# Optimization experiments

Hardware: AMD Instinct MI355X
Metric: run time of the kernel (lower is better)

The kernel has to match this reference:

```python
import jax, jax.numpy as jnp
import numpy as np

B, S, D = 2, 2048, 1024
H, E = 16, 64


def setup_inputs() -> dict:
    key = jax.random.key(0)
    k1, k2, k3, k4 = jax.random.split(key, 4)
    x = jax.random.normal(k1, (B, S, D), dtype=jnp.float32)
    # per-head Q/K/V projection weights, stacked over the head axis
    scale = 1.0 / np.sqrt(D)
    Wq = jax.random.normal(k2, (H, D, E), dtype=jnp.float32) * scale
    Wk = jax.random.normal(k3, (H, D, E), dtype=jnp.float32) * scale
    Wv = jax.random.normal(k4, (H, D, E), dtype=jnp.float32) * scale
    return {"x": x, "Wq": Wq, "Wk": Wk, "Wv": Wv}


def reference(x, Wq, Wk, Wv):
    # Grouped-over-heads equivalent of the per-head torch loop.
    q = jnp.einsum("bsd,hde->bhse", x, Wq)  # [B,H,S,E]
    k = jnp.einsum("bsd,hde->bhse", x, Wk)
    v = jnp.einsum("bsd,hde->bhse", x, Wv)

    scores = jnp.einsum("bhse,bhte->bhst", q, k)  # [B,H,S,S]
    scores = scores / jnp.sqrt(jnp.asarray(E, dtype=scores.dtype))
    causal = jnp.tril(jnp.ones((S, S), dtype=bool))  # True on/below diagonal
    scores = jnp.where(causal, scores, jnp.finfo(scores.dtype).min)
    attn = jax.nn.softmax(scores, axis=-1)  # dropout p=0.0 -> identity

    out = jnp.einsum("bhst,bhte->bhse", attn, v)  # [B,H,S,E]
    # concat over heads on the last dim, matching torch.concat(..., dim=-1)
    return out.transpose(0, 2, 1, 3).reshape(B, S, H * E)
```

## Files before the change

kernel.cpp:

```cpp
#include <hip/hip_runtime.h>
#include <stdint.h>

#define S_LEN 2048
#define D_DIM 1024
#define NB 2
#define NH 16
#define NE 64
#define M_ROWS (NB * S_LEN)
#define N_COLS (3 * NH * NE)
#define K_DIM D_DIM

typedef unsigned short u16;
typedef unsigned int u32;
typedef u16 u16x8 __attribute__((ext_vector_type(8)));
typedef __bf16 bf16x8 __attribute__((ext_vector_type(8)));
typedef float f32x4 __attribute__((ext_vector_type(4)));

__device__ __forceinline__ u16 f2b(float f) {
  u32 u = __builtin_bit_cast(u32, f);
  return (u16)((u + 0x7FFFu + ((u >> 16) & 1u)) >> 16);
}

__device__ __forceinline__ void gload_lds16(const void* g, void* l) {
  __builtin_amdgcn_global_load_lds(
      (const __attribute__((address_space(1))) u32*)g,
      (__attribute__((address_space(3))) u32*)l, 16, 0, 0);
}

__global__ __launch_bounds__(256) void k_prep(const float* __restrict__ x,
                                              const float* __restrict__ Wq,
                                              const float* __restrict__ Wk,
                                              const float* __restrict__ Wv,
                                              u16* __restrict__ xb,
                                              u16* __restrict__ Wt) {
  __shared__ u16 tile[64][65];
  int bid = blockIdx.x;
  int t = threadIdx.x;
  if (bid < 2048) {
    size_t i = (size_t)bid * 256 + t;
    const float4* xf = (const float4*)x;
    float4 a = xf[2 * i], c = xf[2 * i + 1];
    u16x8 o;
    o[0] = f2b(a.x); o[1] = f2b(a.y); o[2] = f2b(a.z); o[3] = f2b(a.w);
    o[4] = f2b(c.x); o[5] = f2b(c.y); o[6] = f2b(c.z); o[7] = f2b(c.w);
    *(u16x8*)(xb + 8 * i) = o;
  } else {
    int wbid = bid - 2048;
    int kb = wbid & 15;
    int h = (wbid >> 4) & 15;
    int proj = wbid >> 8;
    const float* W = (proj == 0) ? Wq : ((proj == 1) ? Wk : Wv);
    int k0 = kb * 64;
    int e = t & 63, kr = t >> 6;
    const float* src = W + ((size_t)h * D_DIM + k0 + kr * 16) * NE + e;
#pragma unroll
    for (int j = 0; j < 16; ++j) tile[kr * 16 + j][e] = f2b(src[(size_t)j * NE]);
    __syncthreads();
    int e2 = t >> 2, kc = (t & 3) * 16;
    u16x8 o0, o1;
#pragma unroll
    for (int j = 0; j < 8; ++j) { o0[j] = tile[kc + j][e2]; o1[j] = tile[kc + 8 + j][e2]; }
    size_t n = (size_t)proj * 1024 + h * 64 + e2;
    u16* dst = Wt + n * K_DIM + k0 + kc;
    *(u16x8*)dst = o0;
    *(u16x8*)(dst + 8) = o1;
  }
}

__global__ __launch_bounds__(256) void k_gemm(const u16* __restrict__ A,
                                              const u16* __restrict__ Bt,
                                              u16* __restrict__ C) {
  __shared__ __align__(16) u16 As[128 * 64];
  __shared__ __align__(16) u16 Bs[128 * 64];
  int t = threadIdx.x;
  int lane = t & 63, w = t >> 6;
  int wr = (w >> 1) * 64, wc = (w & 1) * 64;
  int bid = blockIdx.x;
  int xcd = bid & 7, r0 = bid >> 3;
  int m0 = (r0 / 3) * 128;
  int n0 = (xcd * 3 + (r0 % 3)) * 128;
  float qscale = ((n0 + wc) < 1024) ? 0.18033688f : 1.0f;
  f32x4 acc[4][4];
#pragma unroll
  for (int m = 0; m < 4; m++)
#pragma unroll
    for (int n = 0; n < 4; n++)
#pragma unroll
      for (int j = 0; j < 4; j++) acc[m][n][j] = 0.f;

  for (int k0 = 0; k0 < K_DIM; k0 += 64) {
#pragma unroll
    for (int i = 0; i < 4; ++i) {
      int ci = i * 256 + t;
      int row = ci >> 3, c = ci & 7;
      int cs = c ^ (row & 7);
      gload_lds16(A + (size_t)(m0 + row) * K_DIM + k0 + cs * 8,
                  (char*)As + (size_t)(i * 256 + w * 64) * 16);
      gload_lds16(Bt + (size_t)(n0 + row) * K_DIM + k0 + cs * 8,
                  (char*)Bs + (size_t)(i * 256 + w * 64) * 16);
    }
    __syncthreads();
#pragma unroll
    for (int ks = 0; ks < 2; ++ks) {
      int kc = ks * 4 + (lane >> 4);
      bf16x8 af[4], bfr[4];
#pragma unroll
      for (int m = 0; m < 4; m++) {
        int r = wr + m * 16 + (lane & 15);
        af[m] = *(const bf16x8*)&As[r * 64 + ((kc ^ (r & 7)) * 8)];
      }
#pragma unroll
      for (int n = 0; n < 4; n++) {
        int r = wc + n * 16 + (lane & 15);
        bfr[n] = *(const bf16x8*)&Bs[r * 64 + ((kc ^ (r & 7)) * 8)];
      }
#pragma unroll
      for (int m = 0; m < 4; m++)
#pragma unroll
        for (int n = 0; n < 4; n++)
          acc[m][n] = __builtin_amdgcn_mfma_f32_16x16x32_bf16(af[m], bfr[n], acc[m][n], 0, 0, 0);
    }
    __syncthreads();
  }
#pragma unroll
  for (int m = 0; m < 4; m++) {
#pragma unroll
    for (int r = 0; r < 4; r++) {
      int row = m0 + wr + m * 16 + (lane >> 4) * 4 + r;
#pragma unroll
      for (int n = 0; n < 4; n++) {
        int col = n0 + wc + n * 16 + (lane & 15);
        C[(size_t)row * N_COLS + col] = f2b(acc[m][n][r] * qscale);
      }
    }
  }
}

__device__ __forceinline__ void stage_k(const u16* kb_, u16* kdst, int kv0, int t) {
  int row = t >> 3, c = t & 7;
  int cs = c ^ (row & 7);
  gload_lds16(kb_ + (size_t)(kv0 + row) * N_COLS + cs * 8,
              (char*)kdst + (size_t)t * 16);
}

__device__ __forceinline__ void vwrite(u16* vt, u16x8 va, u16x8 vb2, int vp, int vec) {
#pragma unroll
  for (int j = 0; j < 8; ++j) {
    int e = vec * 8 + j;
    int slot = (vp >> 2) ^ (e & 7) ^ (e >> 3);
    *(u32*)((char*)vt + e * 128 + slot * 16 + (vp & 3) * 4) =
        (u32)va[j] | ((u32)vb2[j] << 16);
  }
}

__global__ __launch_bounds__(512) void k_attn(const u16* __restrict__ qkv,
                                              float* __restrict__ out) {
  __shared__ __align__(16) u16 Ks[2][64 * 64];
  __shared__ __align__(16) u16 Vt[2][64 * 64];
  __shared__ __align__(16) u16 Ps[128 * 64];
  int t = threadIdx.x;
  int lane = t & 63, w = t >> 6;
  int bid = blockIdx.x;
  int xcd = bid & 7, g = bid >> 3;
  int bh = xcd * 4 + (g & 3);
  int qb = 15 - (g >> 2);
  int b = bh >> 4, h = bh & 15;
  const u16* qb_ = qkv + (size_t)b * S_LEN * N_COLS + h * NE;
  const u16* kb_ = qb_ + 1024;
  const u16* vb_ = qb_ + 2048;
  int vp = t >> 3, vec = t & 7;

  int q0 = qb * 128;
  int nt = 2 * qb + 2;

  int qrow = q0 + w * 16 + (lane & 15);
  bf16x8 qf[2];
#pragma unroll
  for (int ks = 0; ks < 2; ks++)
    qf[ks] = *(const bf16x8*)(qb_ + (size_t)qrow * N_COLS + ks * 32 + (lane >> 4) * 8);

  f32x4 o[4];
#pragma unroll
  for (int i = 0; i < 4; i++)
#pragma unroll
    for (int j = 0; j < 4; j++) o[i][j] = 0.f;
  float lrow[4];
#pragma unroll
  for (int r = 0; r < 4; r++) lrow[r] = 0.f;
  int myq = q0 + w * 16 + (lane >> 4) * 4;

  stage_k(kb_, Ks[0], 0, t);
  if (t < 256) {
    const u16* vs = vb_ + (size_t)(2 * vp) * N_COLS + vec * 8;
    u16x8 va = *(const u16x8*)vs;
    u16x8 vb2 = *(const u16x8*)(vs + N_COLS);
    vwrite(Vt[0], va, vb2, vp, vec);
  }
  __syncthreads();

  int cur = 0;
  for (int ti = 0; ti < nt; ++ti) {
    int kv0 = ti * 64;
    bool pf = (ti + 1 < nt);
    u16x8 va, vb2;
    if (pf) {
      if (t < 256) {
        const u16* vs = vb_ + (size_t)(kv0 + 64 + 2 * vp) * N_COLS + vec * 8;
        va = *(const u16x8*)vs;
        vb2 = *(const u16x8*)(vs + N_COLS);
      }
      stage_k(kb_, Ks[cur ^ 1], kv0 + 64, t);
    }

    f32x4 s[4];
#pragma unroll
    for (int f = 0; f < 4; f++)
#pragma unroll
      for (int j = 0; j < 4; j++) s[f][j] = 0.f;
    __builtin_amdgcn_s_setprio(1);
#pragma unroll
    for (int ks = 0; ks < 2; ks++) {
      int kc = ks * 4 + (lane >> 4);
#pragma unroll
      for (int f = 0; f < 4; f++) {
        int r = f * 16 + (lane & 15);
        bf16x8 kf = *(const bf16x8*)&Ks[cur][r * 64 + ((kc ^ (r & 7)) * 8)];
        s[f] = __builtin_amdgcn_mfma_f32_16x16x32_bf16(qf[ks], kf, s[f], 0, 0, 0);
      }
    }
    __builtin_amdgcn_s_setprio(0);

    bool mask = (ti >= nt - 2);
#pragma unroll
    for (int r = 0; r < 4; ++r) {
#pragma unroll
      for (int f = 0; f < 4; f++) {
        float p = __builtin_amdgcn_exp2f(s[f][r]);
        if (mask) {
          int kv = kv0 + f * 16 + (lane & 15);
          p = (kv <= myq + r) ? p : 0.f;
        }
        s[f][r] = p;
      }
      lrow[r] += (s[0][r] + s[1][r]) + (s[2][r] + s[3][r]);
    }

#pragma unroll
    for (int f = 0; f < 4; f++) {
#pragma unroll
      for (int r = 0; r < 4; r++) {
        int row = w * 16 + (lane >> 4) * 4 + r;
        int col = f * 16 + (lane & 15);
        int swz = (col >> 3) ^ (row & 7);
        *(u16*)((char*)Ps + row * 128 + swz * 16 + (col & 7) * 2) =
            __builtin_bit_cast(u16, (__bf16)s[f][r]);
      }
    }

    if (pf && t < 256) vwrite(Vt[cur ^ 1], va, vb2, vp, vec);

    __builtin_amdgcn_s_setprio(1);
#pragma unroll
    for (int ks = 0; ks < 2; ks++) {
      int kc = ks * 4 + (lane >> 4);
      int pr = w * 16 + (lane & 15);
      bf16x8 pa = *(const bf16x8*)&Ps[pr * 64 + ((kc ^ (pr & 7)) * 8)];
#pragma unroll
      for (int ef = 0; ef < 4; ef++) {
        int vr = ef * 16 + (lane & 15);
        int vswz = kc ^ (vr & 7) ^ (vr >> 3);
        bf16x8 vbf = *(const bf16x8*)&Vt[cur][vr * 64 + vswz * 8];
        o[ef] = __builtin_amdgcn_mfma_f32_16x16x32_bf16(pa, vbf, o[ef], 0, 0, 0);
      }
    }
    __builtin_amdgcn_s_setprio(0);
    __syncthreads();
    cur ^= 1;
  }

#pragma unroll
  for (int r = 0; r < 4; r++) {
    float l = lrow[r];
    l += __shfl_xor(l, 1);
    l += __shfl_xor(l, 2);
    l += __shfl_xor(l, 4);
    l += __shfl_xor(l, 8);
    float inv = 1.0f / l;
    int q = myq + r;
#pragma unroll
    for (int ef = 0; ef < 4; ef++) {
      int col = h * NE + ef * 16 + (lane & 15);
      out[((size_t)b * S_LEN + q) * (NH * NE) + col] = o[ef][r] * inv;
    }
  }
}

extern "C" void kernel_launch(void* const* d_in, const int* in_sizes, int n_in,
                              void* d_out, int out_size, void* d_ws, size_t ws_size,
                              hipStream_t stream) {
  const float* x = (const float*)d_in[0];
  const float* Wq = (const float*)d_in[1];
  const float* Wk = (const float*)d_in[2];
  const float* Wv = (const float*)d_in[3];
  float* out = (float*)d_out;

  char* ws = (char*)d_ws;
  u16* xb = (u16*)ws;
  u16* Wt = (u16*)(ws + (8u << 20));
  u16* qkv = (u16*)(ws + (14u << 20));

  k_prep<<<dim3(2816), dim3(256), 0, stream>>>(x, Wq, Wk, Wv, xb, Wt);
  k_gemm<<<dim3(768), dim3(256), 0, stream>>>(xb, Wt, qkv);
  k_attn<<<dim3(512), dim3(512), 0, stream>>>(qkv, out);
}
```

Before: 100.3 us.

## Switch attention to 32x32x16 MFMA with 4 waves and causal tile skipping

Restructures the attention kernel from 8 waves of 16 query rows using 16x16x32 MFMA to 4 waves of 32 query rows using 32x32x16 MFMA. Each wave now has its own P buffer, all 256 threads stage K and V, and waves skip KV tiles lying entirely above their causal diagonal. Masking is applied per wave only on tiles that straddle the diagonal. The larger MFMA shape gives more reuse per LDS fragment load, in exchange for more accumulator registers and half as many waves per block.

```diff
diff --git a/kernel.cpp b/kernel.cpp
--- a/kernel.cpp
+++ b/kernel.cpp
@@ -6,7 +6,6 @@
 #define NB 2
 #define NH 16
 #define NE 64
-#define M_ROWS (NB * S_LEN)
 #define N_COLS (3 * NH * NE)
 #define K_DIM D_DIM
 
@@ -15,6 +14,7 @@
 typedef u16 u16x8 __attribute__((ext_vector_type(8)));
 typedef __bf16 bf16x8 __attribute__((ext_vector_type(8)));
 typedef float f32x4 __attribute__((ext_vector_type(4)));
+typedef float f32x16 __attribute__((ext_vector_type(16)));
 
 __device__ __forceinline__ u16 f2b(float f) {
   u32 u = __builtin_bit_cast(u32, f);
@@ -137,10 +137,14 @@
 }
 
 __device__ __forceinline__ void stage_k(const u16* kb_, u16* kdst, int kv0, int t) {
-  int row = t >> 3, c = t & 7;
-  int cs = c ^ (row & 7);
-  gload_lds16(kb_ + (size_t)(kv0 + row) * N_COLS + cs * 8,
-              (char*)kdst + (size_t)t * 16);
+#pragma unroll
+  for (int i = 0; i < 2; ++i) {
+    int ci = i * 256 + t;
+    int row = ci >> 3, c = ci & 7;
+    int cs = c ^ (row & 7);
+    gload_lds16(kb_ + (size_t)(kv0 + row) * N_COLS + cs * 8,
+                (char*)kdst + (size_t)ci * 16);
+  }
 }
 
 __device__ __forceinline__ void vwrite(u16* vt, u16x8 va, u16x8 vb2, int vp, int vec) {
@@ -153,13 +157,14 @@
   }
 }
 
-__global__ __launch_bounds__(512) void k_attn(const u16* __restrict__ qkv,
-                                              float* __restrict__ out) {
+__global__ __launch_bounds__(256, 3) void k_attn(const u16* __restrict__ qkv,
+                                                 float* __restrict__ out) {
   __shared__ __align__(16) u16 Ks[2][64 * 64];
   __shared__ __align__(16) u16 Vt[2][64 * 64];
-  __shared__ __align__(16) u16 Ps[128 * 64];
+  __shared__ __align__(16) u16 Ps[4][32 * 64];
   int t = threadIdx.x;
   int lane = t & 63, w = t >> 6;
+  int half = lane >> 5, l31 = lane & 31;
   int bid = blockIdx.x;
   int xcd = bid & 7, g = bid >> 3;
   int bh = xcd * 4 + (g & 3);
@@ -172,25 +177,24 @@
 
   int q0 = qb * 128;
   int nt = 2 * qb + 2;
-
-  int qrow = q0 + w * 16 + (lane & 15);
-  bf16x8 qf[2];
-#pragma unroll
-  for (int ks = 0; ks < 2; ks++)
-    qf[ks] = *(const bf16x8*)(qb_ + (size_t)qrow * N_COLS + ks * 32 + (lane >> 4) * 8);
-
-  f32x4 o[4];
-#pragma unroll
-  for (int i = 0; i < 4; i++)
-#pragma unroll
-    for (int j = 0; j < 4; j++) o[i][j] = 0.f;
-  float lrow[4];
-#pragma unroll
-  for (int r = 0; r < 4; r++) lrow[r] = 0.f;
-  int myq = q0 + w * 16 + (lane >> 4) * 4;
+  int wqb = q0 + w * 32;
+
+  bf16x8 qf[4];
+#pragma unroll
+  for (int ks = 0; ks < 4; ks++)
+    qf[ks] = *(const bf16x8*)(qb_ + (size_t)(wqb + l31) * N_COLS + ks * 16 + half * 8);
+
+  f32x16 o[2];
+  float lrow[16];
+#pragma unroll
+  for (int n2 = 0; n2 < 2; n2++)
+#pragma unroll
+    for (int r = 0; r < 16; r++) o[n2][r] = 0.f;
+#pragma unroll
+  for (int r = 0; r < 16; r++) lrow[r] = 0.f;
 
   stage_k(kb_, Ks[0], 0, t);
-  if (t < 256) {
+  {
     const u16* vs = vb_ + (size_t)(2 * vp) * N_COLS + vec * 8;
     u16x8 va = *(const u16x8*)vs;
     u16x8 vb2 = *(const u16x8*)(vs + N_COLS);
@@ -204,93 +208,100 @@
     bool pf = (ti + 1 < nt);
     u16x8 va, vb2;
     if (pf) {
-      if (t < 256) {
-        const u16* vs = vb_ + (size_t)(kv0 + 64 + 2 * vp) * N_COLS + vec * 8;
-        va = *(const u16x8*)vs;
-        vb2 = *(const u16x8*)(vs + N_COLS);
-      }
+      const u16* vs = vb_ + (size_t)(kv0 + 64 + 2 * vp) * N_COLS + vec * 8;
+      va = *(const u16x8*)vs;
+      vb2 = *(const u16x8*)(vs + N_COLS);
       stage_k(kb_, Ks[cur ^ 1], kv0 + 64, t);
     }
 
-    f32x4 s[4];
-#pragma unroll
-    for (int f = 0; f < 4; f++)
-#pragma unroll
-      for (int j = 0; j < 4; j++) s[f][j] = 0.f;
-    __builtin_amdgcn_s_setprio(1);
-#pragma unroll
-    for (int ks = 0; ks < 2; ks++) {
-      int kc = ks * 4 + (lane >> 4);
-#pragma unroll
-      for (int f = 0; f < 4; f++) {
-        int r = f * 16 + (lane & 15);
-        bf16x8 kf = *(const bf16x8*)&Ks[cur][r * 64 + ((kc ^ (r & 7)) * 8)];
-        s[f] = __builtin_amdgcn_mfma_f32_16x16x32_bf16(qf[ks], kf, s[f], 0, 0, 0);
-      }
-    }
-    __builtin_amdgcn_s_setprio(0);
-
-    bool mask = (ti >= nt - 2);
-#pragma unroll
-    for (int r = 0; r < 4; ++r) {
-#pragma unroll
-      for (int f = 0; f < 4; f++) {
-        float p = __builtin_amdgcn_exp2f(s[f][r]);
-        if (mask) {
-          int kv = kv0 + f * 16 + (lane & 15);
-          p = (kv <= myq + r) ? p : 0.f;
+    bool doWork = (kv0 <= wqb + 31);
+    bool needMask = (kv0 + 63 > wqb);
+
+    if (doWork) {
+      f32x16 s[2];
+#pragma unroll
+      for (int n2 = 0; n2 < 2; n2++)
+#pragma unroll
+        for (int r = 0; r < 16; r++) s[n2][r] = 0.f;
+      __builtin_amdgcn_s_setprio(1);
+#pragma unroll
+      for (int ks = 0; ks < 4; ks++) {
+#pragma unroll
+        for (int n2 = 0; n2 < 2; n2++) {
+          int kr = n2 * 32 + l31;
+          int c = (ks * 2 + half) ^ (kr & 7);
+          bf16x8 kf = *(const bf16x8*)&Ks[cur][kr * 64 + c * 8];
+          s[n2] = __builtin_amdgcn_mfma_f32_32x32x16_bf16(qf[ks], kf, s[n2], 0, 0, 0);
         }
-        s[f][r] = p;
-      }
-      lrow[r] += (s[0][r] + s[1][r]) + (s[2][r] + s[3][r]);
-    }
-
-#pragma unroll
-    for (int f = 0; f < 4; f++) {
-#pragma unroll
-      for (int r = 0; r < 4; r++) {
-        int row = w * 16 + (lane >> 4) * 4 + r;
-        int col = f * 16 + (lane & 15);
-        int swz = (col >> 3) ^ (row & 7);
-        *(u16*)((char*)Ps + row * 128 + swz * 16 + (col & 7) * 2) =
-            __builtin_bit_cast(u16, (__bf16)s[f][r]);
-      }
-    }
-
-    if (pf && t < 256) vwrite(Vt[cur ^ 1], va, vb2, vp, vec);
-
-    __builtin_amdgcn_s_setprio(1);
-#pragma unroll
-    for (int ks = 0; ks < 2; ks++) {
-      int kc = ks * 4 + (lane >> 4);
-      int pr = w * 16 + (lane & 15);
-      bf16x8 pa = *(const bf16x8*)&Ps[pr * 64 + ((kc ^ (pr & 7)) * 8)];
-#pragma unroll
-      for (int ef = 0; ef < 4; ef++) {
-        int vr = ef * 16 + (lane & 15);
-        int vswz = kc ^ (vr & 7) ^ (vr >> 3);
-        bf16x8 vbf = *(const bf16x8*)&Vt[cur][vr * 64 + vswz * 8];
-        o[ef] = __builtin_amdgcn_mfma_f32_16x16x32_bf16(pa, vbf, o[ef], 0, 0, 0);
-      }
-    }
-    __builtin_amdgcn_s_setprio(0);
+      }
+      __builtin_amdgcn_s_setprio(0);
+
+#pragma unroll
+      for (int r = 0; r < 16; r++) {
+        int rowq = (r & 3) + 8 * (r >> 2) + 4 * half;
+#pragma unroll
+        for (int n2 = 0; n2 < 2; n2++) {
+          float p = __builtin_amdgcn_exp2f(s[n2][r]);
+          if (needMask) {
+            int kv = kv0 + n2 * 32 + l31;
+            p = (kv <= wqb + rowq) ? p : 0.f;
+          }
+          s[n2][r] = p;
+          lrow[r] += p;
+        }
+      }
+
+#pragma unroll
+      for (int r = 0; r < 16; r++) {
+        int row = (r & 3) + 8 * (r >> 2) + 4 * half;
+#pragma unroll
+        for (int n2 = 0; n2 < 2; n2++) {
+          int col = n2 * 32 + l31;
+          int swz = (col >> 3) ^ (row & 7);
+          *(u16*)((char*)Ps + w * 4096 + row * 128 + swz * 16 + (col & 7) * 2) =
+              __builtin_bit_cast(u16, (__bf16)s[n2][r]);
+        }
+      }
+    }
+
+    if (pf) vwrite(Vt[cur ^ 1], va, vb2, vp, vec);
+
+    if (doWork) {
+      __builtin_amdgcn_s_setprio(1);
+#pragma unroll
+      for (int ks = 0; ks < 4; ks++) {
+        int c2 = ks * 2 + half;
+        bf16x8 pa = *(const bf16x8*)((char*)Ps + w * 4096 + l31 * 128 +
+                                     ((c2 ^ (l31 & 7)) * 16));
+        int kvb = ks * 16 + half * 8;
+#pragma unroll
+        for (int n2 = 0; n2 < 2; n2++) {
+          int e = n2 * 32 + l31;
+          int slot = (kvb >> 3) ^ (e & 7) ^ (e >> 3);
+          bf16x8 vbf = *(const bf16x8*)((char*)Vt[cur] + e * 128 + slot * 16);
+          o[n2] = __builtin_amdgcn_mfma_f32_32x32x16_bf16(pa, vbf, o[n2], 0, 0, 0);
+        }
+      }
+      __builtin_amdgcn_s_setprio(0);
+    }
     __syncthreads();
     cur ^= 1;
   }
 
 #pragma unroll
-  for (int r = 0; r < 4; r++) {
+  for (int r = 0; r < 16; r++) {
     float l = lrow[r];
     l += __shfl_xor(l, 1);
     l += __shfl_xor(l, 2);
     l += __shfl_xor(l, 4);
     l += __shfl_xor(l, 8);
+    l += __shfl_xor(l, 16);
     float inv = 1.0f / l;
-    int q = myq + r;
-#pragma unroll
-    for (int ef = 0; ef < 4; ef++) {
-      int col = h * NE + ef * 16 + (lane & 15);
-      out[((size_t)b * S_LEN + q) * (NH * NE) + col] = o[ef][r] * inv;
+    int q = wqb + (r & 3) + 8 * (r >> 2) + 4 * half;
+#pragma unroll
+    for (int n2 = 0; n2 < 2; n2++) {
+      int col = h * NE + n2 * 32 + l31;
+      out[((size_t)b * S_LEN + q) * (NH * NE) + col] = o[n2][r] * inv;
     }
   }
 }
@@ -311,5 +322,5 @@
 
   k_prep<<<dim3(2816), dim3(256), 0, stream>>>(x, Wq, Wk, Wv, xb, Wt);
   k_gemm<<<dim3(768), dim3(256), 0, stream>>>(xb, Wt, qkv);
-  k_attn<<<dim3(512), dim3(512), 0, stream>>>(qkv, out);
-}
+  k_attn<<<dim3(512), dim3(256), 0, stream>>>(qkv, out);
+}
```

Result: slower. 151.9 us (+51.5%).

## Halve attention block to 4 waves, each owning two 16-row query tiles

Applied to the files above, without the earlier changes.

The attention kernel drops from 8 waves to 4 waves per block. Each wave now handles two 16-row query tiles, 64 rows apart, and reuses each K fragment read from LDS for both tiles. Wave A skips its work on the final KV tile, which lies entirely above its causal diagonal. Each wave now needs more registers (two accumulators and two score sets), and a block has fewer waves to hide latency. The P buffer in shared memory shrinks and is reused by the two tiles in turn.

```diff
diff --git a/kernel.cpp b/kernel.cpp
--- a/kernel.cpp
+++ b/kernel.cpp
@@ -6,7 +6,6 @@
 #define NB 2
 #define NH 16
 #define NE 64
-#define M_ROWS (NB * S_LEN)
 #define N_COLS (3 * NH * NE)
 #define K_DIM D_DIM
 
@@ -136,11 +135,15 @@
   }
 }
 
-__device__ __forceinline__ void stage_k(const u16* kb_, u16* kdst, int kv0, int t) {
-  int row = t >> 3, c = t & 7;
-  int cs = c ^ (row & 7);
-  gload_lds16(kb_ + (size_t)(kv0 + row) * N_COLS + cs * 8,
-              (char*)kdst + (size_t)t * 16);
+__device__ __forceinline__ void stage_k(const u16* kb_, u16* kdst, int kv0, int t, int w) {
+#pragma unroll
+  for (int i = 0; i < 2; ++i) {
+    int ci = i * 256 + t;
+    int row = ci >> 3, c = ci & 7;
+    int cs = c ^ (row & 7);
+    gload_lds16(kb_ + (size_t)(kv0 + row) * N_COLS + cs * 8,
+                (char*)kdst + (size_t)(i * 256 + w * 64) * 16);
+  }
 }
 
 __device__ __forceinline__ void vwrite(u16* vt, u16x8 va, u16x8 vb2, int vp, int vec) {
@@ -153,11 +156,11 @@
   }
 }
 
-__global__ __launch_bounds__(512) void k_attn(const u16* __restrict__ qkv,
+__global__ __launch_bounds__(256) void k_attn(const u16* __restrict__ qkv,
                                               float* __restrict__ out) {
   __shared__ __align__(16) u16 Ks[2][64 * 64];
   __shared__ __align__(16) u16 Vt[2][64 * 64];
-  __shared__ __align__(16) u16 Ps[128 * 64];
+  __shared__ __align__(16) u16 Ps[64 * 64];
   int t = threadIdx.x;
   int lane = t & 63, w = t >> 6;
   int bid = blockIdx.x;
@@ -172,25 +175,27 @@
 
   int q0 = qb * 128;
   int nt = 2 * qb + 2;
-
-  int qrow = q0 + w * 16 + (lane & 15);
-  bf16x8 qf[2];
-#pragma unroll
-  for (int ks = 0; ks < 2; ks++)
-    qf[ks] = *(const bf16x8*)(qb_ + (size_t)qrow * N_COLS + ks * 32 + (lane >> 4) * 8);
-
-  f32x4 o[4];
-#pragma unroll
-  for (int i = 0; i < 4; i++)
-#pragma unroll
-    for (int j = 0; j < 4; j++) o[i][j] = 0.f;
-  float lrow[4];
-#pragma unroll
-  for (int r = 0; r < 4; r++) lrow[r] = 0.f;
-  int myq = q0 + w * 16 + (lane >> 4) * 4;
-
-  stage_k(kb_, Ks[0], 0, t);
-  if (t < 256) {
+  int wqbA = q0 + w * 16;
+
+  bf16x8 qfA[2], qfB[2];
+#pragma unroll
+  for (int ks = 0; ks < 2; ks++) {
+    qfA[ks] = *(const bf16x8*)(qb_ + (size_t)(wqbA + (lane & 15)) * N_COLS + ks * 32 + (lane >> 4) * 8);
+    qfB[ks] = *(const bf16x8*)(qb_ + (size_t)(wqbA + 64 + (lane & 15)) * N_COLS + ks * 32 + (lane >> 4) * 8);
+  }
+
+  f32x4 oA[4], oB[4];
+  float lA[4], lB[4];
+#pragma unroll
+  for (int i = 0; i < 4; i++) {
+#pragma unroll
+    for (int j = 0; j < 4; j++) { oA[i][j] = 0.f; oB[i][j] = 0.f; }
+    lA[i] = 0.f; lB[i] = 0.f;
+  }
+  int myqA = wqbA + (lane >> 4) * 4;
+
+  stage_k(kb_, Ks[0], 0, t, w);
+  {
     const u16* vs = vb_ + (size_t)(2 * vp) * N_COLS + vec * 8;
     u16x8 va = *(const u16x8*)vs;
     u16x8 vb2 = *(const u16x8*)(vs + N_COLS);
@@ -204,19 +209,20 @@
     bool pf = (ti + 1 < nt);
     u16x8 va, vb2;
     if (pf) {
-      if (t < 256) {
-        const u16* vs = vb_ + (size_t)(kv0 + 64 + 2 * vp) * N_COLS + vec * 8;
-        va = *(const u16x8*)vs;
-        vb2 = *(const u16x8*)(vs + N_COLS);
-      }
-      stage_k(kb_, Ks[cur ^ 1], kv0 + 64, t);
-    }
-
-    f32x4 s[4];
+      const u16* vs = vb_ + (size_t)(kv0 + 64 + 2 * vp) * N_COLS + vec * 8;
+      va = *(const u16x8*)vs;
+      vb2 = *(const u16x8*)(vs + N_COLS);
+      stage_k(kb_, Ks[cur ^ 1], kv0 + 64, t, w);
+    }
+    bool doA = (ti != nt - 1);
+    bool maskA = (ti == nt - 2);
+    bool maskB = (ti == nt - 1);
+
+    f32x4 sA[4], sB[4];
 #pragma unroll
     for (int f = 0; f < 4; f++)
 #pragma unroll
-      for (int j = 0; j < 4; j++) s[f][j] = 0.f;
+      for (int j = 0; j < 4; j++) { sA[f][j] = 0.f; sB[f][j] = 0.f; }
     __builtin_amdgcn_s_setprio(1);
 #pragma unroll
     for (int ks = 0; ks < 2; ks++) {
@@ -225,26 +231,70 @@
       for (int f = 0; f < 4; f++) {
         int r = f * 16 + (lane & 15);
         bf16x8 kf = *(const bf16x8*)&Ks[cur][r * 64 + ((kc ^ (r & 7)) * 8)];
-        s[f] = __builtin_amdgcn_mfma_f32_16x16x32_bf16(qf[ks], kf, s[f], 0, 0, 0);
+        sA[f] = __builtin_amdgcn_mfma_f32_16x16x32_bf16(qfA[ks], kf, sA[f], 0, 0, 0);
+        sB[f] = __builtin_amdgcn_mfma_f32_16x16x32_bf16(qfB[ks], kf, sB[f], 0, 0, 0);
       }
     }
     __builtin_amdgcn_s_setprio(0);
 
-    bool mask = (ti >= nt - 2);
+    if (doA) {
+#pragma unroll
+      for (int r = 0; r < 4; ++r) {
+#pragma unroll
+        for (int f = 0; f < 4; f++) {
+          float p = __builtin_amdgcn_exp2f(sA[f][r]);
+          if (maskA) {
+            int kv = kv0 + f * 16 + (lane & 15);
+            p = (kv <= myqA + r) ? p : 0.f;
+          }
+          sA[f][r] = p;
+        }
+        lA[r] += (sA[0][r] + sA[1][r]) + (sA[2][r] + sA[3][r]);
+      }
+#pragma unroll
+      for (int f = 0; f < 4; f++) {
+#pragma unroll
+        for (int r = 0; r < 4; r++) {
+          int row = w * 16 + (lane >> 4) * 4 + r;
+          int col = f * 16 + (lane & 15);
+          int swz = (col >> 3) ^ (row & 7);
+          *(u16*)((char*)Ps + row * 128 + swz * 16 + (col & 7) * 2) =
+              __builtin_bit_cast(u16, (__bf16)sA[f][r]);
+        }
+      }
+      if (pf) vwrite(Vt[cur ^ 1], va, vb2, vp, vec);
+      __builtin_amdgcn_s_setprio(1);
+#pragma unroll
+      for (int ks = 0; ks < 2; ks++) {
+        int kc = ks * 4 + (lane >> 4);
+        int pr = w * 16 + (lane & 15);
+        bf16x8 pa = *(const bf16x8*)&Ps[pr * 64 + ((kc ^ (pr & 7)) * 8)];
+#pragma unroll
+        for (int ef = 0; ef < 4; ef++) {
+          int vr = ef * 16 + (lane & 15);
+          int vswz = kc ^ (vr & 7) ^ (vr >> 3);
+          bf16x8 vbf = *(const bf16x8*)&Vt[cur][vr * 64 + vswz * 8];
+          oA[ef] = __builtin_amdgcn_mfma_f32_16x16x32_bf16(pa, vbf, oA[ef], 0, 0, 0);
+        }
+      }
+      __builtin_amdgcn_s_setprio(0);
+    } else if (pf) {
+      vwrite(Vt[cur ^ 1], va, vb2, vp, vec);
+    }
+
 #pragma unroll
     for (int r = 0; r < 4; ++r) {
 #pragma unroll
       for (int f = 0; f < 4; f++) {
-        float p = __builtin_amdgcn_exp2f(s[f][r]);
-        if (mask) {
+        float p = __builtin_amdgcn_exp2f(sB[f][r]);
+        if (maskB) {
           int kv = kv0 + f * 16 + (lane & 15);
-          p = (kv <= myq + r) ? p : 0.f;
+          p = (kv <= myqA + 64 + r) ? p : 0.f;
         }
-        s[f][r] = p;
-      }
-      lrow[r] += (s[0][r] + s[1][r]) + (s[2][r] + s[3][r]);
-    }
-
+        sB[f][r] = p;
+      }
+      lB[r] += (sB[0][r] + sB[1][r]) + (sB[2][r] + sB[3][r]);
+    }
 #pragma unroll
     for (int f = 0; f < 4; f++) {
 #pragma unroll
@@ -253,12 +303,9 @@
         int col = f * 16 + (lane & 15);
         int swz = (col >> 3) ^ (row & 7);
         *(u16*)((char*)Ps + row * 128 + swz * 16 + (col & 7) * 2) =
-            __builtin_bit_cast(u16, (__bf16)s[f][r]);
-      }
-    }
-
-    if (pf && t < 256) vwrite(Vt[cur ^ 1], va, vb2, vp, vec);
-
+            __builtin_bit_cast(u16, (__bf16)sB[f][r]);
+      }
+    }
     __builtin_amdgcn_s_setprio(1);
 #pragma unroll
     for (int ks = 0; ks < 2; ks++) {
@@ -270,7 +317,7 @@
         int vr = ef * 16 + (lane & 15);
         int vswz = kc ^ (vr & 7) ^ (vr >> 3);
         bf16x8 vbf = *(const bf16x8*)&Vt[cur][vr * 64 + vswz * 8];
-        o[ef] = __builtin_amdgcn_mfma_f32_16x16x32_bf16(pa, vbf, o[ef], 0, 0, 0);
+        oB[ef] = __builtin_amdgcn_mfma_f32_16x16x32_bf16(pa, vbf, oB[ef], 0, 0, 0);
       }
     }
     __builtin_amdgcn_s_setprio(0);
@@ -280,17 +327,19 @@
 
 #pragma unroll
   for (int r = 0; r < 4; r++) {
-    float l = lrow[r];
-    l += __shfl_xor(l, 1);
-    l += __shfl_xor(l, 2);
-    l += __shfl_xor(l, 4);
-    l += __shfl_xor(l, 8);
-    float inv = 1.0f / l;
-    int q = myq + r;
+    float la = lA[r], lb = lB[r];
+    la += __shfl_xor(la, 1); lb += __shfl_xor(lb, 1);
+    la += __shfl_xor(la, 2); lb += __shfl_xor(lb, 2);
+    la += __shfl_xor(la, 4); lb += __shfl_xor(lb, 4);
+    la += __shfl_xor(la, 8); lb += __shfl_xor(lb, 8);
+    float invA = 1.0f / la, invB = 1.0f / lb;
+    int qA = myqA + r;
 #pragma unroll
     for (int ef = 0; ef < 4; ef++) {
       int col = h * NE + ef * 16 + (lane & 15);
-      out[((size_t)b * S_LEN + q) * (NH * NE) + col] = o[ef][r] * inv;
+      size_t base = (size_t)b * S_LEN;
+      out[(base + qA) * (NH * NE) + col] = oA[ef][r] * invA;
+      out[(base + qA + 64) * (NH * NE) + col] = oB[ef][r] * invB;
     }
   }
 }
@@ -311,5 +360,5 @@
 
   k_prep<<<dim3(2816), dim3(256), 0, stream>>>(x, Wq, Wk, Wv, xb, Wt);
   k_gemm<<<dim3(768), dim3(256), 0, stream>>>(xb, Wt, qkv);
-  k_attn<<<dim3(512), dim3(512), 0, stream>>>(qkv, out);
-}
+  k_attn<<<dim3(512), dim3(256), 0, stream>>>(qkv, out);
+}
```

Result: slower. 119.3 us (+18.9%).
